# Performance work log

Measured on AMD Instinct MI355X. Metric: run time of the kernel, lower is better.

## Reference

```python
import jax, jax.numpy as jnp
import numpy as np

B, C, H, W = 64, 1, 1024, 1024
NEG_WEIGHT = 0.1  # constant loss contribution where target != 1


def setup_inputs() -> dict:
    key = jax.random.key(0)
    k1, k2 = jax.random.split(key)
    prediction = jax.random.normal(k1, (B, C, H, W), dtype=jnp.float32)
    target = jax.random.randint(k2, (B, C, H, W), 0, 2, dtype=jnp.int32)
    return {"prediction": prediction, "target": target}


def reference(prediction, target):
    # loss_i = 1 - sigmoid(pred_i) if target_i == 1 else 0.1; return mean over all elements
    p = jax.nn.sigmoid(prediction)
    loss = jnp.where(target == 1, 1.0 - p, jnp.float32(NEG_WEIGHT))
    return jnp.mean(loss)
```

## Files before the change

kernel.cpp:

```cpp
#include <hip/hip_runtime.h>


__global__ __launch_bounds__(256)
void wloss_kernel(const float* __restrict__ pred,
                  const int*   __restrict__ tgt,
                  float* __restrict__ out,
                  long long n, float inv_n) {
    const long long n4     = n >> 2;
    const long long tid    = (long long)blockIdx.x * blockDim.x + threadIdx.x;
    const long long stride = (long long)gridDim.x * blockDim.x;

    const float4* __restrict__ p4 = (const float4*)pred;
    const int4*   __restrict__ t4 = (const int4*)tgt;

    float acc = 0.0f;
    for (long long i = tid; i < n4; i += stride) {
        float4 p = p4[i];
        int4   t = t4[i];
        float l0 = (t.x == 1) ? 1.0f / (1.0f + __expf(p.x)) : 0.1f;
        float l1 = (t.y == 1) ? 1.0f / (1.0f + __expf(p.y)) : 0.1f;
        float l2 = (t.z == 1) ? 1.0f / (1.0f + __expf(p.z)) : 0.1f;
        float l3 = (t.w == 1) ? 1.0f / (1.0f + __expf(p.w)) : 0.1f;
        acc += (l0 + l1) + (l2 + l3);
    }

    if (blockIdx.x == 0) {
        for (long long i = (n4 << 2) + threadIdx.x; i < n; i += blockDim.x) {
            acc += (tgt[i] == 1) ? 1.0f / (1.0f + __expf(pred[i])) : 0.1f;
        }
    }

    #pragma unroll
    for (int off = 32; off > 0; off >>= 1)
        acc += __shfl_down(acc, off, 64);

    __shared__ float smem[4];
    const int lane = threadIdx.x & 63;
    const int wave = threadIdx.x >> 6;
    if (lane == 0) smem[wave] = acc;
    __syncthreads();
    if (threadIdx.x == 0) {
        float bsum = (smem[0] + smem[1]) + (smem[2] + smem[3]);
        atomicAdd(out, bsum * inv_n);
    }
}

extern "C" void kernel_launch(void* const* d_in, const int* in_sizes, int n_in,
                              void* d_out, int out_size, void* d_ws, size_t ws_size,
                              hipStream_t stream) {
    const float* pred = (const float*)d_in[0];
    const int*   tgt  = (const int*)d_in[1];
    float*       out  = (float*)d_out;

    const long long n = (long long)in_sizes[0];

    hipMemsetAsync(out, 0, sizeof(float), stream);

    const int block = 256;
    const long long n4 = n >> 2;
    long long g = (n4 + block - 1) / block;
    if (g > 8192) g = 8192;
    if (g < 1)    g = 1;

    wloss_kernel<<<(int)g, block, 0, stream>>>(pred, tgt, out, n, 1.0f / (float)n);
}
```

Before: 537.4 us.

## Add software-pipelined fast path with fixed grid and prefetch two iterations ahead

Adds a specialised kernel for sizes that divide evenly into a 2048x256 grid stride. It keeps two iterations of float4/int4 loads in flight ahead of the compute, uses int indexing, and drops the bounds checks and the tail handling. The grid shrinks from 8192 to 2048 blocks, so each thread does more iterations. The goal is to hide memory latency in a bandwidth-bound reduction, at the cost of higher register use per thread.

```diff
diff --git a/kernel.cpp b/kernel.cpp
--- a/kernel.cpp
+++ b/kernel.cpp
@@ -1,40 +1,22 @@
 #include <hip/hip_runtime.h>
 
 
-__global__ __launch_bounds__(256)
-void wloss_kernel(const float* __restrict__ pred,
-                  const int*   __restrict__ tgt,
-                  float* __restrict__ out,
-                  long long n, float inv_n) {
-    const long long n4     = n >> 2;
-    const long long tid    = (long long)blockIdx.x * blockDim.x + threadIdx.x;
-    const long long stride = (long long)gridDim.x * blockDim.x;
+#define BLOCK 256
 
-    const float4* __restrict__ p4 = (const float4*)pred;
-    const int4*   __restrict__ t4 = (const int4*)tgt;
+__device__ __forceinline__ float loss4(float4 p, int4 t) {
+    float l0 = (t.x == 1) ? 1.0f / (1.0f + __expf(p.x)) : 0.1f;
+    float l1 = (t.y == 1) ? 1.0f / (1.0f + __expf(p.y)) : 0.1f;
+    float l2 = (t.z == 1) ? 1.0f / (1.0f + __expf(p.z)) : 0.1f;
+    float l3 = (t.w == 1) ? 1.0f / (1.0f + __expf(p.w)) : 0.1f;
+    return (l0 + l1) + (l2 + l3);
+}
 
-    float acc = 0.0f;
-    for (long long i = tid; i < n4; i += stride) {
-        float4 p = p4[i];
-        int4   t = t4[i];
-        float l0 = (t.x == 1) ? 1.0f / (1.0f + __expf(p.x)) : 0.1f;
-        float l1 = (t.y == 1) ? 1.0f / (1.0f + __expf(p.y)) : 0.1f;
-        float l2 = (t.z == 1) ? 1.0f / (1.0f + __expf(p.z)) : 0.1f;
-        float l3 = (t.w == 1) ? 1.0f / (1.0f + __expf(p.w)) : 0.1f;
-        acc += (l0 + l1) + (l2 + l3);
-    }
-
-    if (blockIdx.x == 0) {
-        for (long long i = (n4 << 2) + threadIdx.x; i < n; i += blockDim.x) {
-            acc += (tgt[i] == 1) ? 1.0f / (1.0f + __expf(pred[i])) : 0.1f;
-        }
-    }
-
-    #pragma unroll
+__device__ __forceinline__ void block_reduce_atomic(float acc, float inv_n,
+                                                    float* __restrict__ out) {
+#pragma unroll
     for (int off = 32; off > 0; off >>= 1)
         acc += __shfl_down(acc, off, 64);
-
-    __shared__ float smem[4];
+    __shared__ float smem[BLOCK / 64];
     const int lane = threadIdx.x & 63;
     const int wave = threadIdx.x >> 6;
     if (lane == 0) smem[wave] = acc;
@@ -45,6 +27,54 @@
     }
 }
 
+__global__ __launch_bounds__(BLOCK)
+void wloss_pipe(const float4* __restrict__ p4,
+                const int4*   __restrict__ t4,
+                float* __restrict__ out,
+                int iters, int stride, float inv_n) {
+    int i = blockIdx.x * BLOCK + threadIdx.x;
+
+    float4 pA = p4[i];          int4 tA = t4[i];
+    float4 pB = p4[i + stride]; int4 tB = t4[i + stride];
+    int idx = i + 2 * stride;
+
+    float acc = 0.0f;
+    for (int k = 0; k < iters - 2; ++k) {
+        float4 pN = p4[idx];
+        int4   tN = t4[idx];
+        idx += stride;
+        acc += loss4(pA, tA);
+        pA = pB; tA = tB;
+        pB = pN; tB = tN;
+    }
+    acc += loss4(pA, tA);
+    acc += loss4(pB, tB);
+
+    block_reduce_atomic(acc, inv_n, out);
+}
+
+__global__ __launch_bounds__(BLOCK)
+void wloss_generic(const float* __restrict__ pred,
+                   const int*   __restrict__ tgt,
+                   float* __restrict__ out,
+                   long long n, float inv_n) {
+    const long long n4     = n >> 2;
+    const long long tid    = (long long)blockIdx.x * blockDim.x + threadIdx.x;
+    const long long stride = (long long)gridDim.x * blockDim.x;
+
+    const float4* p4 = (const float4*)pred;
+    const int4*   t4 = (const int4*)tgt;
+
+    float acc = 0.0f;
+    for (long long i = tid; i < n4; i += stride)
+        acc += loss4(p4[i], t4[i]);
+    if (blockIdx.x == 0) {
+        for (long long i = (n4 << 2) + threadIdx.x; i < n; i += blockDim.x)
+            acc += (tgt[i] == 1) ? 1.0f / (1.0f + __expf(pred[i])) : 0.1f;
+    }
+    block_reduce_atomic(acc, inv_n, out);
+}
+
 extern "C" void kernel_launch(void* const* d_in, const int* in_sizes, int n_in,
                               void* d_out, int out_size, void* d_ws, size_t ws_size,
                               hipStream_t stream) {
@@ -53,14 +83,23 @@
     float*       out  = (float*)d_out;
 
     const long long n = (long long)in_sizes[0];
+    const float inv_n = 1.0f / (float)n;
 
     hipMemsetAsync(out, 0, sizeof(float), stream);
 
-    const int block = 256;
     const long long n4 = n >> 2;
-    long long g = (n4 + block - 1) / block;
-    if (g > 8192) g = 8192;
-    if (g < 1)    g = 1;
+    const int grid = 2048;
+    const long long stride = (long long)grid * BLOCK;
 
-    wloss_kernel<<<(int)g, block, 0, stream>>>(pred, tgt, out, n, 1.0f / (float)n);
+    if ((n & 3) == 0 && n4 % stride == 0 && n4 / stride >= 2) {
+        const int iters = (int)(n4 / stride);
+        wloss_pipe<<<grid, BLOCK, 0, stream>>>((const float4*)pred,
+                                               (const int4*)tgt, out,
+                                               iters, (int)stride, inv_n);
+    } else {
+        long long g = (n4 + BLOCK - 1) / BLOCK;
+        if (g > 8192) g = 8192;
+        if (g < 1)    g = 1;
+        wloss_generic<<<(int)g, BLOCK, 0, stream>>>(pred, tgt, out, n, inv_n);
+    }
 }
```

After: 506.5 us. 5.8% less time.
